# Performance work log

Hardware: AMD Instinct MI355X
Metric: run time of the kernel (lower is better)

Reference implementation:

```python
import jax, jax.numpy as jnp
import numpy as np

NEG_SLOPE = 0.2
EPS = 1e-16


def gat_conv(x, src, dst, W, att_src, att_dst, bias, heads, out_ch):
    """PyG-style GATConv. src/dst already include self-loops. Messages flow src -> dst."""
    N = x.shape[0]
    h = (x @ W).reshape(N, heads, out_ch)          # [N, H, C]
    a_src = jnp.sum(h * att_src, axis=-1)          # [N, H]
    a_dst = jnp.sum(h * att_dst, axis=-1)          # [N, H]
    e = a_src[src] + a_dst[dst]                    # [E, H]
    e = jax.nn.leaky_relu(e, NEG_SLOPE)
    # softmax over incoming edges per destination node
    m = jax.ops.segment_max(e, dst, num_segments=N)      # [N, H]
    m = jnp.where(jnp.isfinite(m), m, 0.0)
    ex = jnp.exp(e - m[dst])                       # [E, H]
    denom = jax.ops.segment_sum(ex, dst, num_segments=N)  # [N, H]
    alpha = ex / (denom[dst] + EPS)                # [E, H]
    msg = alpha[:, :, None] * h[src]               # [E, H, C]
    out = jax.ops.segment_sum(msg, dst, num_segments=N)   # [N, H, C]
    return out, bias


def add_self_loops(edge_index, N):
    loop = jnp.arange(N, dtype=edge_index.dtype)
    src = jnp.concatenate([edge_index[0], loop])
    dst = jnp.concatenate([edge_index[1], loop])
    return src, dst


def setup_inputs() -> dict:
    key = jax.random.key(0)
    ks = jax.random.split(key, 10)
    N, E, IN, HID, OUT, H = 100000, 1600000, 128, 32, 32, 4
    s = lambda fan: 1.0 / np.sqrt(fan)
    return {
        "x": jax.random.normal(ks[0], (N, IN), dtype=jnp.float32),
        "edge_index": jax.random.randint(ks[1], (2, E), 0, N, dtype=jnp.int32),
        "W1": jax.random.normal(ks[2], (IN, H * HID), dtype=jnp.float32) * s(IN),
        "att_src1": jax.random.normal(ks[3], (H, HID), dtype=jnp.float32) * s(HID),
        "att_dst1": jax.random.normal(ks[4], (H, HID), dtype=jnp.float32) * s(HID),
        "b1": jnp.zeros((H * HID,), dtype=jnp.float32),
        "W2": jax.random.normal(ks[5], (H * HID, OUT), dtype=jnp.float32) * s(H * HID),
        "att_src2": jax.random.normal(ks[6], (1, OUT), dtype=jnp.float32) * s(OUT),
        "att_dst2": jax.random.normal(ks[7], (1, OUT), dtype=jnp.float32) * s(OUT),
        "b2": jnp.zeros((OUT,), dtype=jnp.float32),
    }


def reference(x, edge_index, W1, att_src1, att_dst1, b1, W2, att_src2, att_dst2, b2):
    N = x.shape[0]
    src, dst = add_self_loops(edge_index, N)
    # layer 1: 4 heads, concat=True
    out1, bias1 = gat_conv(x, src, dst, W1, att_src1, att_dst1, b1, heads=4, out_ch=32)
    h1 = jax.nn.relu(out1.reshape(N, -1) + bias1)          # [N, 128]
    # layer 2: 1 head, concat=False (mean over 1 head == squeeze)
    out2, bias2 = gat_conv(h1, src, dst, W2, att_src2, att_dst2, b2, heads=1, out_ch=32)
    return out2.mean(axis=1) + bias2                       # [N, 32]
```

## Files before the change

kernel.cpp:

```cpp
#include <hip/hip_runtime.h>
#include <hip/hip_bf16.h>


typedef __bf16 bf16x8 __attribute__((ext_vector_type(8)));
typedef float f32x4 __attribute__((ext_vector_type(4)));

__device__ __forceinline__ float lrelu(float v) { return v >= 0.f ? v : 0.2f * v; }

__device__ __forceinline__ unsigned f2bf(float f) {
    unsigned u = __float_as_uint(f);
    return (u + 0x7FFFu + ((u >> 16) & 1u)) >> 16;
}

__device__ __forceinline__ bf16x8 as_bf16x8(uint4 u) {
    union { uint4 u; bf16x8 b; } c; c.u = u; return c.b;
}

__device__ __forceinline__ void bf16x8_fma(uint4 hv, float a, float* acc) {
    acc[0] = fmaf(a, __uint_as_float(hv.x << 16), acc[0]);
    acc[1] = fmaf(a, __uint_as_float(hv.x & 0xFFFF0000u), acc[1]);
    acc[2] = fmaf(a, __uint_as_float(hv.y << 16), acc[2]);
    acc[3] = fmaf(a, __uint_as_float(hv.y & 0xFFFF0000u), acc[3]);
    acc[4] = fmaf(a, __uint_as_float(hv.z << 16), acc[4]);
    acc[5] = fmaf(a, __uint_as_float(hv.z & 0xFFFF0000u), acc[5]);
    acc[6] = fmaf(a, __uint_as_float(hv.w << 16), acc[6]);
    acc[7] = fmaf(a, __uint_as_float(hv.w & 0xFFFF0000u), acc[7]);
}

__global__ __launch_bounds__(256) void cast_w_k(const float* __restrict__ W1,
                                                const float* __restrict__ W2,
                                                ushort* __restrict__ w1t,
                                                ushort* __restrict__ w2t) {
    int tid = blockIdx.x * 256 + threadIdx.x;
    if (tid < 16384) {
        int k = tid >> 7, c = tid & 127;
        w1t[c * 128 + k] = (ushort)f2bf(W1[tid]);
    }
    if (tid < 4096) {
        int k = tid >> 5, c = tid & 31;
        w2t[c * 128 + k] = (ushort)f2bf(W2[tid]);
    }
}

__global__ __launch_bounds__(256) void gemm1_mfma(
    const float* __restrict__ x, const ushort* __restrict__ w1t,
    const float* __restrict__ atts, const float* __restrict__ attd,
    ushort* __restrict__ h, float* __restrict__ as_, float* __restrict__ ad_, int N) {
    const int w = threadIdx.x >> 6;
    const int l = threadIdx.x & 63;
    const int c15 = l & 15;
    const int quad = l >> 4;
    const int n_base = blockIdx.x * 64 + w * 16;
    const int n = n_base + c15;

    bf16x8 a[4];
    if (n < N) {
        const float4* xr = (const float4*)(x + (size_t)n * 128);
#pragma unroll
        for (int ks = 0; ks < 4; ks++) {
            float4 p0 = xr[ks * 8 + quad * 2];
            float4 p1 = xr[ks * 8 + quad * 2 + 1];
            uint4 u;
            u.x = f2bf(p0.x) | (f2bf(p0.y) << 16);
            u.y = f2bf(p0.z) | (f2bf(p0.w) << 16);
            u.z = f2bf(p1.x) | (f2bf(p1.y) << 16);
            u.w = f2bf(p1.z) | (f2bf(p1.w) << 16);
            a[ks] = as_bf16x8(u);
        }
    } else {
        uint4 z = make_uint4(0, 0, 0, 0);
#pragma unroll
        for (int ks = 0; ks < 4; ks++) a[ks] = as_bf16x8(z);
    }

    f32x4 acc[8];
#pragma unroll
    for (int ct = 0; ct < 8; ct++) acc[ct] = (f32x4){0.f, 0.f, 0.f, 0.f};

#pragma unroll
    for (int ct = 0; ct < 8; ct++) {
        const uint4* wr = (const uint4*)(w1t + (size_t)(ct * 16 + c15) * 128);
#pragma unroll
        for (int ks = 0; ks < 4; ks++) {
            bf16x8 bfrag = as_bf16x8(wr[ks * 4 + quad]);
            acc[ct] = __builtin_amdgcn_mfma_f32_16x16x32_bf16(a[ks], bfrag, acc[ct], 0, 0, 0);
        }
    }

#pragma unroll
    for (int ct = 0; ct < 8; ct++) {
        int col = ct * 16 + c15;
#pragma unroll
        for (int reg = 0; reg < 4; reg++) {
            int n_out = n_base + quad * 4 + reg;
            if (n_out < N) h[(size_t)n_out * 128 + col] = (ushort)f2bf(acc[ct][reg]);
        }
    }
#pragma unroll
    for (int hh = 0; hh < 4; hh++) {
        float sA = atts[hh * 32 + c15], sB = atts[hh * 32 + 16 + c15];
        float dA = attd[hh * 32 + c15], dB = attd[hh * 32 + 16 + c15];
#pragma unroll
        for (int reg = 0; reg < 4; reg++) {
            float ps = acc[2 * hh][reg] * sA + acc[2 * hh + 1][reg] * sB;
            float pd = acc[2 * hh][reg] * dA + acc[2 * hh + 1][reg] * dB;
            ps += __shfl_xor(ps, 1); pd += __shfl_xor(pd, 1);
            ps += __shfl_xor(ps, 2); pd += __shfl_xor(pd, 2);
            ps += __shfl_xor(ps, 4); pd += __shfl_xor(pd, 4);
            ps += __shfl_xor(ps, 8); pd += __shfl_xor(pd, 8);
            int n_out = n_base + quad * 4 + reg;
            if (c15 == 0 && n_out < N) { as_[n_out * 4 + hh] = ps; ad_[n_out * 4 + hh] = pd; }
        }
    }
}

__global__ __launch_bounds__(256) void gemm2_mfma(
    const ushort* __restrict__ ob, const ushort* __restrict__ w2t,
    const float* __restrict__ atts, const float* __restrict__ attd,
    ushort* __restrict__ h, float* __restrict__ as_, float* __restrict__ ad_, int N) {
    const int w = threadIdx.x >> 6;
    const int l = threadIdx.x & 63;
    const int c15 = l & 15;
    const int quad = l >> 4;
    const int n_base = blockIdx.x * 64 + w * 16;
    const int n = n_base + c15;

    bf16x8 a[4];
    if (n < N) {
        const uint4* xr = (const uint4*)(ob + (size_t)n * 128);
#pragma unroll
        for (int ks = 0; ks < 4; ks++) a[ks] = as_bf16x8(xr[ks * 4 + quad]);
    } else {
        uint4 z = make_uint4(0, 0, 0, 0);
#pragma unroll
        for (int ks = 0; ks < 4; ks++) a[ks] = as_bf16x8(z);
    }

    f32x4 acc[2];
#pragma unroll
    for (int ct = 0; ct < 2; ct++) acc[ct] = (f32x4){0.f, 0.f, 0.f, 0.f};

#pragma unroll
    for (int ct = 0; ct < 2; ct++) {
        const uint4* wr = (const uint4*)(w2t + (size_t)(ct * 16 + c15) * 128);
#pragma unroll
        for (int ks = 0; ks < 4; ks++) {
            bf16x8 bfrag = as_bf16x8(wr[ks * 4 + quad]);
            acc[ct] = __builtin_amdgcn_mfma_f32_16x16x32_bf16(a[ks], bfrag, acc[ct], 0, 0, 0);
        }
    }

#pragma unroll
    for (int ct = 0; ct < 2; ct++) {
        int col = ct * 16 + c15;
#pragma unroll
        for (int reg = 0; reg < 4; reg++) {
            int n_out = n_base + quad * 4 + reg;
            if (n_out < N) h[(size_t)n_out * 32 + col] = (ushort)f2bf(acc[ct][reg]);
        }
    }
    float sA = atts[c15], sB = atts[16 + c15];
    float dA = attd[c15], dB = attd[16 + c15];
#pragma unroll
    for (int reg = 0; reg < 4; reg++) {
        float ps = acc[0][reg] * sA + acc[1][reg] * sB;
        float pd = acc[0][reg] * dA + acc[1][reg] * dB;
        ps += __shfl_xor(ps, 1); pd += __shfl_xor(pd, 1);
        ps += __shfl_xor(ps, 2); pd += __shfl_xor(pd, 2);
        ps += __shfl_xor(ps, 4); pd += __shfl_xor(pd, 4);
        ps += __shfl_xor(ps, 8); pd += __shfl_xor(pd, 8);
        int n_out = n_base + quad * 4 + reg;
        if (c15 == 0 && n_out < N) { as_[n_out] = ps; ad_[n_out] = pd; }
    }
}

__global__ __launch_bounds__(256) void hist_rank_k(const int* __restrict__ ei, int E, int N,
                                                   int* __restrict__ deg, int* __restrict__ rank) {
    int e = blockIdx.x * 256 + threadIdx.x;
    if (e >= E + N) return;
    int d = (e < E) ? ei[E + e] : e - E;
    rank[e] = atomicAdd(&deg[d], 1);
}

__global__ __launch_bounds__(256) void scan1_k(const int* __restrict__ deg,
                                               int* __restrict__ tmp, int* __restrict__ partial, int N) {
    __shared__ int sh[256];
    int i = blockIdx.x * 256 + threadIdx.x;
    int v = (i < N) ? deg[i] : 0;
    sh[threadIdx.x] = v;
    __syncthreads();
#pragma unroll
    for (int off = 1; off < 256; off <<= 1) {
        int t = (threadIdx.x >= off) ? sh[threadIdx.x - off] : 0;
        __syncthreads();
        sh[threadIdx.x] += t;
        __syncthreads();
    }
    if (i < N) tmp[i] = sh[threadIdx.x];
    if (threadIdx.x == 255) partial[blockIdx.x] = sh[255];
}

__global__ __launch_bounds__(1024) void scan2_k(int* __restrict__ partial, int B) {
    __shared__ int sh[1024];
    int i = threadIdx.x;
    int v = (i < B) ? partial[i] : 0;
    sh[i] = v;
    __syncthreads();
#pragma unroll
    for (int off = 1; off < 1024; off <<= 1) {
        int t = (i >= off) ? sh[i - off] : 0;
        __syncthreads();
        sh[i] += t;
        __syncthreads();
    }
    if (i < B) partial[i] = sh[i] - v;
}

__global__ __launch_bounds__(256) void scan3_k(const int* __restrict__ tmp, const int* __restrict__ partial,
                                               int* __restrict__ rs, int N) {
    int i = blockIdx.x * 256 + threadIdx.x;
    if (i < N) rs[i + 1] = tmp[i] + partial[blockIdx.x];
    if (i == 0) rs[0] = 0;
}

__global__ __launch_bounds__(256) void scatter_k(const int* __restrict__ ei, const int* __restrict__ rank,
                                                 const int* __restrict__ rs, int E, int N,
                                                 int* __restrict__ csr) {
    int e = blockIdx.x * 256 + threadIdx.x;
    if (e >= E + N) return;
    int s, d;
    if (e < E) { s = ei[e]; d = ei[E + e]; } else { s = e - E; d = s; }
    csr[rs[d] + rank[e]] = s;
}

__global__ __launch_bounds__(256) void gather1_k(
    const int* __restrict__ rs, const int* __restrict__ csr,
    const float* __restrict__ as_, const float* __restrict__ ad_,
    const uint4* __restrict__ h, const float* __restrict__ b,
    ushort* __restrict__ o, int N) {
    const int jj = threadIdx.x & 31;
    const int l16 = jj & 15;
    const int sub = jj & 16;
    const int d = blockIdx.x * 16 + (threadIdx.x >> 5) * 2 + (jj >> 4);
    if (d >= N) return;
    const int hl = l16 >> 2;
    const int sl = l16 & 3;
    const int beg = rs[d], end = rs[d + 1];
    const float adv = ad_[d * 4 + hl];

    float acc[8];
#pragma unroll
    for (int i = 0; i < 8; i++) acc[i] = 0.f;
    float den = 0.f;

    int j0 = beg;
    int sv0 = 0, sv1 = 0;
    float ex0 = 0.f, ex1 = 0.f;
    bool have = (j0 + 8 <= end);
    if (have) {
        sv0 = csr[j0 + sl];
        sv1 = csr[j0 + sl + 4];
        ex0 = __expf(fminf(lrelu(as_[sv0 * 4 + hl] + adv), 80.f));
        ex1 = __expf(fminf(lrelu(as_[sv1 * 4 + hl] + adv), 80.f));
    }
    while (have) {
        bool nhave = (j0 + 16 <= end);
        int na = nhave ? (j0 + 8) : beg;
        int psv0 = csr[na + sl];
        int psv1 = csr[na + sl + 4];
        den += ex0 + ex1;
        float av[8]; uint4 hv[8];
#pragma unroll
        for (int e = 0; e < 8; e++) {
            const int k = e >> 2, q = e & 3;
            const int srcl = sub + (l16 & 12) + q;
            float exk = k ? ex1 : ex0;
            int   svk = k ? sv1 : sv0;
            av[e] = __shfl(exk, srcl, 32);
            int s = __shfl(svk, srcl, 32);
            hv[e] = h[(size_t)s * 16 + l16];
        }
        float pex0 = __expf(fminf(lrelu(as_[psv0 * 4 + hl] + adv), 80.f));
        float pex1 = __expf(fminf(lrelu(as_[psv1 * 4 + hl] + adv), 80.f));
#pragma unroll
        for (int e = 0; e < 8; e++) bf16x8_fma(hv[e], av[e], acc);
        sv0 = psv0; sv1 = psv1; ex0 = pex0; ex1 = pex1;
        j0 += 8; have = nhave;
    }
    int r = end - j0;
    if (r > 0) {
        float ex0r = 0.f, ex1r = 0.f;
        int   sv0r = 0,   sv1r = 0;
        if (sl < r) {
            sv0r = csr[j0 + sl];
            ex0r = __expf(fminf(lrelu(as_[sv0r * 4 + hl] + adv), 80.f));
            den += ex0r;
        }
        if (sl + 4 < r) {
            sv1r = csr[j0 + sl + 4];
            ex1r = __expf(fminf(lrelu(as_[sv1r * 4 + hl] + adv), 80.f));
            den += ex1r;
        }
        float av[8]; uint4 hv[8];
#pragma unroll
        for (int e = 0; e < 8; e++) {
            const int k = e >> 2, q = e & 3;
            const int srcl = sub + (l16 & 12) + q;
            float exk = k ? ex1r : ex0r;
            int   svk = k ? sv1r : sv0r;
            av[e] = __shfl(exk, srcl, 32);
            int s = __shfl(svk, srcl, 32);
            hv[e] = h[(size_t)s * 16 + l16];
        }
#pragma unroll
        for (int e = 0; e < 8; e++) if (e < r) bf16x8_fma(hv[e], av[e], acc);
    }
    den += __shfl_xor(den, 1, 32);
    den += __shfl_xor(den, 2, 32);
    const float rcp = 1.f / (den + 1e-16f);
    float4 b0 = *(const float4*)&b[l16 * 8];
    float4 b1 = *(const float4*)&b[l16 * 8 + 4];
    float v0 = fmaxf(acc[0] * rcp + b0.x, 0.f);
    float v1 = fmaxf(acc[1] * rcp + b0.y, 0.f);
    float v2 = fmaxf(acc[2] * rcp + b0.z, 0.f);
    float v3 = fmaxf(acc[3] * rcp + b0.w, 0.f);
    float v4 = fmaxf(acc[4] * rcp + b1.x, 0.f);
    float v5 = fmaxf(acc[5] * rcp + b1.y, 0.f);
    float v6 = fmaxf(acc[6] * rcp + b1.z, 0.f);
    float v7 = fmaxf(acc[7] * rcp + b1.w, 0.f);
    uint4 pk;
    pk.x = f2bf(v0) | (f2bf(v1) << 16);
    pk.y = f2bf(v2) | (f2bf(v3) << 16);
    pk.z = f2bf(v4) | (f2bf(v5) << 16);
    pk.w = f2bf(v6) | (f2bf(v7) << 16);
    ((uint4*)o)[(size_t)d * 16 + l16] = pk;
}

__global__ __launch_bounds__(256) void gather2_k(
    const int* __restrict__ rs, const int* __restrict__ csr,
    const float* __restrict__ as_, const float* __restrict__ ad_,
    const uint4* __restrict__ h, const float* __restrict__ b,
    float* __restrict__ o, int N) {
    const int jj = threadIdx.x & 31;
    const int l4 = jj & 3;
    const int sub = jj & 28;
    const int d = blockIdx.x * 64 + (threadIdx.x >> 5) * 8 + (jj >> 2);
    if (d >= N) return;
    const int beg = rs[d], end = rs[d + 1];
    const float adv = ad_[d];

    float acc[8];
#pragma unroll
    for (int i = 0; i < 8; i++) acc[i] = 0.f;
    float den = 0.f;

    int j0 = beg;
    int sv0 = 0, sv1 = 0;
    float ex0 = 0.f, ex1 = 0.f;
    bool have = (j0 + 8 <= end);
    if (have) {
        sv0 = csr[j0 + l4];
        sv1 = csr[j0 + l4 + 4];
        ex0 = __expf(fminf(lrelu(as_[sv0] + adv), 80.f));
        ex1 = __expf(fminf(lrelu(as_[sv1] + adv), 80.f));
    }
    while (have) {
        bool nhave = (j0 + 16 <= end);
        int na = nhave ? (j0 + 8) : beg;
        int psv0 = csr[na + l4];
        int psv1 = csr[na + l4 + 4];
        den += ex0 + ex1;
        float av[8]; uint4 hv[8];
#pragma unroll
        for (int e = 0; e < 8; e++) {
            const int k = e >> 2, q = e & 3;
            const int srcl = sub + q;
            float exk = k ? ex1 : ex0;
            int   svk = k ? sv1 : sv0;
            av[e] = __shfl(exk, srcl, 32);
            int s = __shfl(svk, srcl, 32);
            hv[e] = h[(size_t)s * 4 + l4];
        }
        float pex0 = __expf(fminf(lrelu(as_[psv0] + adv), 80.f));
        float pex1 = __expf(fminf(lrelu(as_[psv1] + adv), 80.f));
#pragma unroll
        for (int e = 0; e < 8; e++) bf16x8_fma(hv[e], av[e], acc);
        sv0 = psv0; sv1 = psv1; ex0 = pex0; ex1 = pex1;
        j0 += 8; have = nhave;
    }
    int r = end - j0;
    if (r > 0) {
        float ex0r = 0.f, ex1r = 0.f;
        int   sv0r = 0,   sv1r = 0;
        if (l4 < r) {
            sv0r = csr[j0 + l4];
            ex0r = __expf(fminf(lrelu(as_[sv0r] + adv), 80.f));
            den += ex0r;
        }
        if (l4 + 4 < r) {
            sv1r = csr[j0 + l4 + 4];
            ex1r = __expf(fminf(lrelu(as_[sv1r] + adv), 80.f));
            den += ex1r;
        }
        float av[8]; uint4 hv[8];
#pragma unroll
        for (int e = 0; e < 8; e++) {
            const int k = e >> 2, q = e & 3;
            const int srcl = sub + q;
            float exk = k ? ex1r : ex0r;
            int   svk = k ? sv1r : sv0r;
            av[e] = __shfl(exk, srcl, 32);
            int s = __shfl(svk, srcl, 32);
            hv[e] = h[(size_t)s * 4 + l4];
        }
#pragma unroll
        for (int e = 0; e < 8; e++) if (e < r) bf16x8_fma(hv[e], av[e], acc);
    }
    den += __shfl_xor(den, 1, 32);
    den += __shfl_xor(den, 2, 32);
    const float rcp = 1.f / (den + 1e-16f);
    float4 b0 = *(const float4*)&b[l4 * 8];
    float4 b1 = *(const float4*)&b[l4 * 8 + 4];
    float4 o0, o1v;
    o0.x  = acc[0] * rcp + b0.x;
    o0.y  = acc[1] * rcp + b0.y;
    o0.z  = acc[2] * rcp + b0.z;
    o0.w  = acc[3] * rcp + b0.w;
    o1v.x = acc[4] * rcp + b1.x;
    o1v.y = acc[5] * rcp + b1.y;
    o1v.z = acc[6] * rcp + b1.z;
    o1v.w = acc[7] * rcp + b1.w;
    *(float4*)&o[(size_t)d * 32 + l4 * 8]     = o0;
    *(float4*)&o[(size_t)d * 32 + l4 * 8 + 4] = o1v;
}

extern "C" void kernel_launch(void* const* d_in, const int* in_sizes, int n_in,
                              void* d_out, int out_size, void* d_ws, size_t ws_size,
                              hipStream_t stream) {
    const float* x    = (const float*)d_in[0];
    const int*   ei   = (const int*)d_in[1];
    const float* W1   = (const float*)d_in[2];
    const float* as1v = (const float*)d_in[3];
    const float* ad1v = (const float*)d_in[4];
    const float* b1   = (const float*)d_in[5];
    const float* W2   = (const float*)d_in[6];
    const float* as2v = (const float*)d_in[7];
    const float* ad2v = (const float*)d_in[8];
    const float* b2   = (const float*)d_in[9];
    float* out = (float*)d_out;

    const int N = in_sizes[0] / 128;
    const int E = in_sizes[1] / 2;
    const int EN = E + N;
    const int B = (N + 255) / 256;

    char* base = (char*)d_ws;
    size_t o = 0;
    auto alloc = [&](size_t bytes) { void* p = base + o; o += (bytes + 255) & ~(size_t)255; return p; };
    ushort* w1t  = (ushort*)alloc((size_t)128 * 128 * 2);
    ushort* w2t  = (ushort*)alloc((size_t)32 * 128 * 2);
    ushort* h1   = (ushort*)alloc((size_t)N * 128 * 2);
    ushort* h2   = (ushort*)alloc((size_t)N * 32 * 2);
    ushort* o1   = (ushort*)alloc((size_t)N * 128 * 2);
    float*  as1  = (float*)alloc((size_t)N * 4 * 4);
    float*  ad1  = (float*)alloc((size_t)N * 4 * 4);
    float*  as2  = (float*)alloc((size_t)N * 4);
    float*  ad2  = (float*)alloc((size_t)N * 4);
    int*    deg  = (int*)alloc((size_t)N * 4);
    int*    tmp  = (int*)alloc((size_t)N * 4);
    int*    part = (int*)alloc((size_t)1024 * 4);
    int*    rs   = (int*)alloc((size_t)(N + 1) * 4);
    int*    rank = (int*)alloc((size_t)EN * 4);
    int*    csr  = (int*)alloc((size_t)EN * 4);

    hipMemsetAsync(deg, 0, (size_t)N * 4, stream);

    const int nbE = (EN + 255) / 256;
    const int nbN = (N + 255) / 256;
    const int nbG = (N + 63) / 64;

    cast_w_k<<<64, 256, 0, stream>>>(W1, W2, w1t, w2t);
    gemm1_mfma<<<nbG, 256, 0, stream>>>(x, w1t, as1v, ad1v, h1, as1, ad1, N);
    hist_rank_k<<<nbE, 256, 0, stream>>>(ei, E, N, deg, rank);
    scan1_k<<<nbN, 256, 0, stream>>>(deg, tmp, part, N);
    scan2_k<<<1, 1024, 0, stream>>>(part, B);
    scan3_k<<<nbN, 256, 0, stream>>>(tmp, part, rs, N);
    scatter_k<<<nbE, 256, 0, stream>>>(ei, rank, rs, E, N, csr);

    gather1_k<<<(N + 15) / 16, 256, 0, stream>>>(rs, csr, as1, ad1, (const uint4*)h1, b1, o1, N);

    gemm2_mfma<<<nbG, 256, 0, stream>>>(o1, w2t, as2v, ad2v, h2, as2, ad2, N);
    gather2_k<<<(N + 63) / 64, 256, 0, stream>>>(rs, csr, as2, ad2, (const uint4*)h2, b2, out, N);
}
```

Baseline: 363.2 us.

## Fuse layer-2 GEMM into gather1 epilogue and merge histogram into gemm1 launch

The layer-1 aggregation now stages each 16-node tile of its output in shared memory, and one wavefront runs the layer-2 MFMA GEMM plus the attention dot products on it. This removes the o1 intermediate round-trip through global memory and the separate gemm2 launch. The degree histogram/rank atomics are also merged into the gemm1 launch as extra blocks, so they can overlap with the GEMM. Edge loads in both gathers are now guarded by the valid count, which avoids wasted gathers. The costs are a block-wide barrier and a serial GEMM tail running on only 64 of 256 threads in gather1, plus extra shared memory.

```diff
diff --git a/kernel.cpp b/kernel.cpp
--- a/kernel.cpp
+++ b/kernel.cpp
@@ -42,10 +42,20 @@
     }
 }
 
-__global__ __launch_bounds__(256) void gemm1_mfma(
+__global__ __launch_bounds__(256) void gemm1_hist_k(
     const float* __restrict__ x, const ushort* __restrict__ w1t,
     const float* __restrict__ atts, const float* __restrict__ attd,
-    ushort* __restrict__ h, float* __restrict__ as_, float* __restrict__ ad_, int N) {
+    ushort* __restrict__ h, float* __restrict__ as_, float* __restrict__ ad_,
+    const int* __restrict__ ei, int* __restrict__ deg, int* __restrict__ rank,
+    int N, int E, int nbG) {
+    if (blockIdx.x >= nbG) {
+        int e = (blockIdx.x - nbG) * 256 + threadIdx.x;
+        if (e < E + N) {
+            int d = (e < E) ? ei[E + e] : e - E;
+            rank[e] = atomicAdd(&deg[d], 1);
+        }
+        return;
+    }
     const int w = threadIdx.x >> 6;
     const int l = threadIdx.x & 63;
     const int c15 = l & 15;
@@ -114,74 +124,6 @@
     }
 }
 
-__global__ __launch_bounds__(256) void gemm2_mfma(
-    const ushort* __restrict__ ob, const ushort* __restrict__ w2t,
-    const float* __restrict__ atts, const float* __restrict__ attd,
-    ushort* __restrict__ h, float* __restrict__ as_, float* __restrict__ ad_, int N) {
-    const int w = threadIdx.x >> 6;
-    const int l = threadIdx.x & 63;
-    const int c15 = l & 15;
-    const int quad = l >> 4;
-    const int n_base = blockIdx.x * 64 + w * 16;
-    const int n = n_base + c15;
-
-    bf16x8 a[4];
-    if (n < N) {
-        const uint4* xr = (const uint4*)(ob + (size_t)n * 128);
-#pragma unroll
-        for (int ks = 0; ks < 4; ks++) a[ks] = as_bf16x8(xr[ks * 4 + quad]);
-    } else {
-        uint4 z = make_uint4(0, 0, 0, 0);
-#pragma unroll
-        for (int ks = 0; ks < 4; ks++) a[ks] = as_bf16x8(z);
-    }
-
-    f32x4 acc[2];
-#pragma unroll
-    for (int ct = 0; ct < 2; ct++) acc[ct] = (f32x4){0.f, 0.f, 0.f, 0.f};
-
-#pragma unroll
-    for (int ct = 0; ct < 2; ct++) {
-        const uint4* wr = (const uint4*)(w2t + (size_t)(ct * 16 + c15) * 128);
-#pragma unroll
-        for (int ks = 0; ks < 4; ks++) {
-            bf16x8 bfrag = as_bf16x8(wr[ks * 4 + quad]);
-            acc[ct] = __builtin_amdgcn_mfma_f32_16x16x32_bf16(a[ks], bfrag, acc[ct], 0, 0, 0);
-        }
-    }
-
-#pragma unroll
-    for (int ct = 0; ct < 2; ct++) {
-        int col = ct * 16 + c15;
-#pragma unroll
-        for (int reg = 0; reg < 4; reg++) {
-            int n_out = n_base + quad * 4 + reg;
-            if (n_out < N) h[(size_t)n_out * 32 + col] = (ushort)f2bf(acc[ct][reg]);
-        }
-    }
-    float sA = atts[c15], sB = atts[16 + c15];
-    float dA = attd[c15], dB = attd[16 + c15];
-#pragma unroll
-    for (int reg = 0; reg < 4; reg++) {
-        float ps = acc[0][reg] * sA + acc[1][reg] * sB;
-        float pd = acc[0][reg] * dA + acc[1][reg] * dB;
-        ps += __shfl_xor(ps, 1); pd += __shfl_xor(pd, 1);
-        ps += __shfl_xor(ps, 2); pd += __shfl_xor(pd, 2);
-        ps += __shfl_xor(ps, 4); pd += __shfl_xor(pd, 4);
-        ps += __shfl_xor(ps, 8); pd += __shfl_xor(pd, 8);
-        int n_out = n_base + quad * 4 + reg;
-        if (c15 == 0 && n_out < N) { as_[n_out] = ps; ad_[n_out] = pd; }
-    }
-}
-
-__global__ __launch_bounds__(256) void hist_rank_k(const int* __restrict__ ei, int E, int N,
-                                                   int* __restrict__ deg, int* __restrict__ rank) {
-    int e = blockIdx.x * 256 + threadIdx.x;
-    if (e >= E + N) return;
-    int d = (e < E) ? ei[E + e] : e - E;
-    rank[e] = atomicAdd(&deg[d], 1);
-}
-
 __global__ __launch_bounds__(256) void scan1_k(const int* __restrict__ deg,
                                                int* __restrict__ tmp, int* __restrict__ partial, int N) {
     __shared__ int sh[256];
@@ -237,16 +179,21 @@
     const int* __restrict__ rs, const int* __restrict__ csr,
     const float* __restrict__ as_, const float* __restrict__ ad_,
     const uint4* __restrict__ h, const float* __restrict__ b,
-    ushort* __restrict__ o, int N) {
+    const ushort* __restrict__ w2t, const float* __restrict__ atts2,
+    const float* __restrict__ attd2,
+    ushort* __restrict__ h2, float* __restrict__ as2, float* __restrict__ ad2,
+    int N) {
+    __shared__ uint4 o1s[16][18];
     const int jj = threadIdx.x & 31;
     const int l16 = jj & 15;
     const int sub = jj & 16;
-    const int d = blockIdx.x * 16 + (threadIdx.x >> 5) * 2 + (jj >> 4);
-    if (d >= N) return;
+    const int dl = (threadIdx.x >> 5) * 2 + (jj >> 4);
+    const int d = blockIdx.x * 16 + dl;
     const int hl = l16 >> 2;
     const int sl = l16 & 3;
-    const int beg = rs[d], end = rs[d + 1];
-    const float adv = ad_[d * 4 + hl];
+    int beg = 0, end = 0;
+    float adv = 0.f;
+    if (d < N) { beg = rs[d]; end = rs[d + 1]; adv = ad_[d * 4 + hl]; }
 
     float acc[8];
 #pragma unroll
@@ -310,7 +257,7 @@
             int   svk = k ? sv1r : sv0r;
             av[e] = __shfl(exk, srcl, 32);
             int s = __shfl(svk, srcl, 32);
-            hv[e] = h[(size_t)s * 16 + l16];
+            if (e < r) hv[e] = h[(size_t)s * 16 + l16];
         }
 #pragma unroll
         for (int e = 0; e < 8; e++) if (e < r) bf16x8_fma(hv[e], av[e], acc);
@@ -333,7 +280,52 @@
     pk.y = f2bf(v2) | (f2bf(v3) << 16);
     pk.z = f2bf(v4) | (f2bf(v5) << 16);
     pk.w = f2bf(v6) | (f2bf(v7) << 16);
-    ((uint4*)o)[(size_t)d * 16 + l16] = pk;
+    o1s[dl][l16] = pk;
+    __syncthreads();
+
+    if (threadIdx.x < 64) {
+        const int l = threadIdx.x;
+        const int c15g = l & 15;
+        const int quad = l >> 4;
+        bf16x8 a2[4];
+#pragma unroll
+        for (int ks = 0; ks < 4; ks++) a2[ks] = as_bf16x8(o1s[c15g][ks * 4 + quad]);
+        f32x4 acc2[2];
+#pragma unroll
+        for (int ct = 0; ct < 2; ct++) acc2[ct] = (f32x4){0.f, 0.f, 0.f, 0.f};
+#pragma unroll
+        for (int ct = 0; ct < 2; ct++) {
+            const uint4* wr = (const uint4*)(w2t + (size_t)(ct * 16 + c15g) * 128);
+#pragma unroll
+            for (int ks = 0; ks < 4; ks++) {
+                bf16x8 bfrag = as_bf16x8(wr[ks * 4 + quad]);
+                acc2[ct] = __builtin_amdgcn_mfma_f32_16x16x32_bf16(a2[ks], bfrag, acc2[ct], 0, 0, 0);
+            }
+        }
+        const int nb = blockIdx.x * 16;
+#pragma unroll
+        for (int ct = 0; ct < 2; ct++) {
+            int col = ct * 16 + c15g;
+#pragma unroll
+            for (int reg = 0; reg < 4; reg++) {
+                int n_out = nb + quad * 4 + reg;
+                if (n_out < N) h2[(size_t)n_out * 32 + col] = (ushort)f2bf(acc2[ct][reg]);
+            }
+        }
+        float sA = atts2[c15g], sB = atts2[16 + c15g];
+        float dA = attd2[c15g], dB = attd2[16 + c15g];
+#pragma unroll
+        for (int reg = 0; reg < 4; reg++) {
+            float ps = acc2[0][reg] * sA + acc2[1][reg] * sB;
+            float pd = acc2[0][reg] * dA + acc2[1][reg] * dB;
+            ps += __shfl_xor(ps, 1); pd += __shfl_xor(pd, 1);
+            ps += __shfl_xor(ps, 2); pd += __shfl_xor(pd, 2);
+            ps += __shfl_xor(ps, 4); pd += __shfl_xor(pd, 4);
+            ps += __shfl_xor(ps, 8); pd += __shfl_xor(pd, 8);
+            int n_out = nb + quad * 4 + reg;
+            if (c15g == 0 && n_out < N) { as2[n_out] = ps; ad2[n_out] = pd; }
+        }
+    }
 }
 
 __global__ __launch_bounds__(256) void gather2_k(
@@ -411,7 +403,7 @@
             int   svk = k ? sv1r : sv0r;
             av[e] = __shfl(exk, srcl, 32);
             int s = __shfl(svk, srcl, 32);
-            hv[e] = h[(size_t)s * 4 + l4];
+            if (e < r) hv[e] = h[(size_t)s * 4 + l4];
         }
 #pragma unroll
         for (int e = 0; e < 8; e++) if (e < r) bf16x8_fma(hv[e], av[e], acc);
@@ -461,7 +453,6 @@
     ushort* w2t  = (ushort*)alloc((size_t)32 * 128 * 2);
     ushort* h1   = (ushort*)alloc((size_t)N * 128 * 2);
     ushort* h2   = (ushort*)alloc((size_t)N * 32 * 2);
-    ushort* o1   = (ushort*)alloc((size_t)N * 128 * 2);
     float*  as1  = (float*)alloc((size_t)N * 4 * 4);
     float*  ad1  = (float*)alloc((size_t)N * 4 * 4);
     float*  as2  = (float*)alloc((size_t)N * 4);
@@ -480,15 +471,15 @@
     const int nbG = (N + 63) / 64;
 
     cast_w_k<<<64, 256, 0, stream>>>(W1, W2, w1t, w2t);
-    gemm1_mfma<<<nbG, 256, 0, stream>>>(x, w1t, as1v, ad1v, h1, as1, ad1, N);
-    hist_rank_k<<<nbE, 256, 0, stream>>>(ei, E, N, deg, rank);
+    gemm1_hist_k<<<nbG + nbE, 256, 0, stream>>>(x, w1t, as1v, ad1v, h1, as1, ad1,
+                                                ei, deg, rank, N, E, nbG);
     scan1_k<<<nbN, 256, 0, stream>>>(deg, tmp, part, N);
     scan2_k<<<1, 1024, 0, stream>>>(part, B);
     scan3_k<<<nbN, 256, 0, stream>>>(tmp, part, rs, N);
     scatter_k<<<nbE, 256, 0, stream>>>(ei, rank, rs, E, N, csr);
 
-    gather1_k<<<(N + 15) / 16, 256, 0, stream>>>(rs, csr, as1, ad1, (const uint4*)h1, b1, o1, N);
-
-    gemm2_mfma<<<nbG, 256, 0, stream>>>(o1, w2t, as2v, ad2v, h2, as2, ad2, N);
+    gather1_k<<<(N + 15) / 16, 256, 0, stream>>>(rs, csr, as1, ad1, (const uint4*)h1, b1,
+                                                 w2t, as2v, ad2v, h2, as2, ad2, N);
+
     gather2_k<<<(N + 63) / 64, 256, 0, stream>>>(rs, csr, as2, ad2, (const uint4*)h2, b2, out, N);
 }
```

After: 347.3 us. 4.4% less time.
